# Kernel tuning notes

Hardware: AMD Instinct MI355X
Metric: run time of the kernel (lower is better)

## Reference

```python
import jax, jax.numpy as jnp
import numpy as np

D = 1024
H = 4096  # int(dim * mlp_ratio)
E = 8
B, N = 2, 2048


def setup_inputs() -> dict:
    key = jax.random.key(0)
    ks = jax.random.split(key, 5)
    x = jax.random.normal(ks[0], (B, N, D), dtype=jnp.float32)
    # torch Linear weights, stored pre-transposed for right-multiplication
    W1 = jax.random.normal(ks[1], (E, D, H), dtype=jnp.float32) / np.sqrt(D)
    W2 = jax.random.normal(ks[2], (E, H, D), dtype=jnp.float32) / np.sqrt(H)
    Wg = jax.random.normal(ks[3], (D, E), dtype=jnp.float32) / np.sqrt(D)
    bg = jax.random.normal(ks[4], (E,), dtype=jnp.float32) * 0.01
    return {"x": x, "W1": W1, "W2": W2, "Wg": Wg, "bg": bg}


def reference(x, W1, W2, Wg, bg):
    b, n, d = x.shape
    e = Wg.shape[1]
    xf = x.reshape(b * n, d)                      # [T, D]
    logits = xf @ Wg + bg                         # [T, E]
    one_hot = jax.nn.one_hot(jnp.argmax(logits, axis=-1), e, dtype=x.dtype)  # [T, E]
    # Dense all-experts compute (faithful to the original module)
    h = jax.nn.gelu(jnp.einsum('td,edh->eth', xf, W1), approximate=True)     # [E, T, H]
    y = jnp.einsum('eth,ehd->etd', h, W2)                                    # [E, T, D]
    out = jnp.einsum('etd,te->td', y, one_hot)                               # top-1 combine
    return out.reshape(b, n, d)
```

## Files before the change

kernel.cpp:

```cpp
#include <hip/hip_runtime.h>
#include <hip/hip_bf16.h>

#define Dq 1024
#define Hq 4096
#define Tq 4096
#define MAXTILES 40
#define BM 128
#define BN 256
#define BK 32

#define XB_OFF 65536
#define HC_OFF (XB_OFF + Tq * Dq * 2)
#define WT_OFF (HC_OFF + MAXTILES * BM * Hq * 2)

#define M_NT 0
#define M_CNT 8
#define M_POFF 16
#define M_CUR 32
#define M_TE 64
#define M_TR 128
#define M_EXP 512
#define M_PERM 4608

typedef __attribute__((ext_vector_type(8))) short bf16x8;
typedef __attribute__((ext_vector_type(4))) float f32x4;

__device__ __forceinline__ short f2bf(float f) {
    __hip_bfloat16 h = __float2bfloat16(f);
    return *reinterpret_cast<short*>(&h);
}

__device__ __forceinline__ float gelu_tanh(float x) {
    float u = 0.7978845608028654f * (x + 0.044715f * x * x * x);
    return x / (1.0f + __expf(-2.0f * u));
}

typedef __attribute__((address_space(1))) const void gvoid;
typedef __attribute__((address_space(3))) void lvoid;
__device__ __forceinline__ void glds16(const void* g, void* l) {
    __builtin_amdgcn_global_load_lds((gvoid*)g, (lvoid*)l, 16, 0, 0);
}

#define WAITVM_(N) asm volatile("s_waitcnt vmcnt(" #N ")" ::: "memory")
#define WAITVM(N) WAITVM_(N)

__global__ void k_init(int* meta) {
    int i = blockIdx.x * 256 + threadIdx.x;
    if (i < M_PERM + MAXTILES * BM) meta[i] = 0;
}

__global__ void k_tr(const float* __restrict__ in, short* __restrict__ out, int R, int C) {
    __shared__ float t[64][65];
    int e = blockIdx.z;
    int c0 = blockIdx.x * 64;
    int r0 = blockIdx.y * 64;
    const float* ine = in + (size_t)e * R * C;
    short* oute = out + (size_t)e * R * C;
    int tt = threadIdx.x;
    int lr = tt >> 4;
    int lc = (tt & 15) * 4;
#pragma unroll
    for (int p = 0; p < 4; ++p) {
        int r = p * 16 + lr;
        float4 v = *(const float4*)(ine + (size_t)(r0 + r) * C + c0 + lc);
        t[r][lc] = v.x; t[r][lc + 1] = v.y; t[r][lc + 2] = v.z; t[r][lc + 3] = v.w;
    }
    __syncthreads();
#pragma unroll
    for (int p = 0; p < 4; ++p) {
        int c = p * 16 + lr;
        short4 s;
        s.x = f2bf(t[lc][c]); s.y = f2bf(t[lc + 1][c]);
        s.z = f2bf(t[lc + 2][c]); s.w = f2bf(t[lc + 3][c]);
        *(short4*)(oute + (size_t)(c0 + c) * R + r0 + lc) = s;
    }
}

__global__ void k_route(const float* __restrict__ x, const float* __restrict__ Wg,
                        const float* __restrict__ bg, int* meta, short* __restrict__ xb) {
    int wave = threadIdx.x >> 6;
    int lane = threadIdx.x & 63;
    int t = blockIdx.x * 4 + wave;
    const float* xr = x + (size_t)t * Dq;
    float acc[8];
#pragma unroll
    for (int e = 0; e < 8; ++e) acc[e] = 0.0f;
#pragma unroll
    for (int j = 0; j < 16; ++j) {
        int d = j * 64 + lane;
        float xv = xr[d];
        xb[(size_t)t * Dq + d] = f2bf(xv);
        float4 w0 = *(const float4*)(Wg + (size_t)d * 8);
        float4 w1 = *(const float4*)(Wg + (size_t)d * 8 + 4);
        acc[0] += xv * w0.x; acc[1] += xv * w0.y; acc[2] += xv * w0.z; acc[3] += xv * w0.w;
        acc[4] += xv * w1.x; acc[5] += xv * w1.y; acc[6] += xv * w1.z; acc[7] += xv * w1.w;
    }
#pragma unroll
    for (int e = 0; e < 8; ++e) {
#pragma unroll
        for (int off = 32; off > 0; off >>= 1) acc[e] += __shfl_xor(acc[e], off);
    }
    if (lane == 0) {
        float best = acc[0] + bg[0];
        int be = 0;
#pragma unroll
        for (int e = 1; e < 8; ++e) {
            float v = acc[e] + bg[e];
            if (v > best) { best = v; be = e; }
        }
        meta[M_EXP + t] = be;
        atomicAdd(&meta[M_CNT + be], 1);
    }
}

__global__ void k_scan(int* meta) {
    if (threadIdx.x != 0) return;
    int off = 0, nt = 0;
    for (int e = 0; e < 8; ++e) {
        meta[M_POFF + e] = off;
        int c = meta[M_CNT + e];
        int m = (c + BM - 1) / BM;
        for (int j = 0; j < m; ++j) {
            meta[M_TE + nt] = e;
            meta[M_TR + nt] = off + j * BM;
            ++nt;
        }
        off += m * BM;
    }
    meta[M_POFF + 8] = off;
    meta[M_NT] = nt;
}

__global__ void k_scatter(int* meta) {
    int t = blockIdx.x * 256 + threadIdx.x;
    if (t >= Tq) return;
    int e = meta[M_EXP + t];
    int pos = atomicAdd(&meta[M_CUR + e], 1);
    meta[M_PERM + meta[M_POFF + e] + pos] = t;
}

#define GSTEP(VMN, DO_ISSUE, KN)                                               \
  {                                                                            \
    if (DO_ISSUE) {                                                            \
      int fA = fill * (BM * BK), fB = fill * (BN * BK);                        \
      glds16(aSrc + (size_t)(KN) * BK, As + fA + tt * 8);                      \
      glds16(bSrc0 + (size_t)(KN) * BK, Bs + fB + tt * 8);                     \
      glds16(bSrc1 + (size_t)(KN) * BK, Bs + fB + 4096 + tt * 8);              \
    }                                                                          \
    WAITVM(VMN);                                                               \
    __builtin_amdgcn_s_barrier();                                              \
    asm volatile("" ::: "memory");                                             \
    __builtin_amdgcn_sched_barrier(0);                                         \
    {                                                                          \
      int cA = cur * (BM * BK), cB = cur * (BN * BK);                          \
      bf16x8 af[4], bfv[4];                                                    \
      _Pragma("unroll")                                                        \
      for (int f = 0; f < 4; ++f) {                                            \
        af[f]  = *(const bf16x8*)(&As[cA + aoff[f]]);                          \
        bfv[f] = *(const bf16x8*)(&Bs[cB + boff[f]]);                          \
      }                                                                        \
      __builtin_amdgcn_s_setprio(1);                                           \
      _Pragma("unroll")                                                        \
      for (int fm = 0; fm < 4; ++fm)                                           \
        _Pragma("unroll")                                                      \
        for (int fn = 0; fn < 4; ++fn)                                         \
          acc[fm][fn] = __builtin_amdgcn_mfma_f32_16x16x32_bf16(               \
              af[fm], bfv[fn], acc[fm][fn], 0, 0, 0);                          \
      __builtin_amdgcn_s_setprio(0);                                           \
    }                                                                          \
    __builtin_amdgcn_s_barrier();                                              \
    asm volatile("" ::: "memory");                                             \
    cur = cur == 2 ? 0 : cur + 1;                                              \
    fill = fill == 2 ? 0 : fill + 1;                                           \
  }

__global__ __launch_bounds__(512, 4) void k_gemm1(const short* __restrict__ xb,
                                                  const short* __restrict__ W1T,
                                                  const int* __restrict__ meta,
                                                  short* __restrict__ Hc) {
    __shared__ short As[3 * BM * BK];
    __shared__ short Bs[3 * BN * BK];
    int lin = blockIdx.x + gridDim.x * blockIdx.y;
    int swzid = (lin & 7) * 80 + (lin >> 3);
    int mt = swzid % MAXTILES;
    int n0 = (swzid / MAXTILES) * BN;
    if (mt >= meta[M_NT]) return;
    int e = meta[M_TE + mt];
    int i0 = meta[M_TR + mt];
    int tt = threadIdx.x;
    int wave = tt >> 6, lane = tt & 63;
    int fr = lane & 15, fg = lane >> 4;
    const int* perm = meta + M_PERM;

    int am = tt >> 2;
    int asw = ((tt & 3) ^ ((am >> 1) & 3)) * 8;
    const short* aSrc = xb + (size_t)perm[i0 + am] * Dq + asw;
    int bn_ = tt >> 2;
    int bsw = ((tt & 3) ^ ((bn_ >> 1) & 3)) * 8;
    const short* bSrc0 = W1T + ((size_t)e * Hq + n0 + bn_) * Dq + bsw;
    const short* bSrc1 = bSrc0 + (size_t)128 * Dq;

    int wm = (wave >> 2) * 64, wn = (wave & 3) * 64;
    int aoff[4], boff[4];
#pragma unroll
    for (int f = 0; f < 4; ++f) {
        int m = wm + f * 16 + fr;
        aoff[f] = m * BK + ((fg ^ ((m >> 1) & 3)) * 8);
        int n = wn + f * 16 + fr;
        boff[f] = n * BK + ((fg ^ ((n >> 1) & 3)) * 8);
    }

    f32x4 acc[4][4];
#pragma unroll
    for (int a = 0; a < 4; ++a)
#pragma unroll
        for (int b = 0; b < 4; ++b) acc[a][b] = (f32x4){0.f, 0.f, 0.f, 0.f};

    glds16(aSrc, As + tt * 8);
    glds16(bSrc0, Bs + tt * 8);
    glds16(bSrc1, Bs + 4096 + tt * 8);
    glds16(aSrc + BK, As + BM * BK + tt * 8);
    glds16(bSrc0 + BK, Bs + BN * BK + tt * 8);
    glds16(bSrc1 + BK, Bs + BN * BK + 4096 + tt * 8);

    int cur = 0, fill = 2;
    for (int i = 0; i < 30; ++i) GSTEP(6, true, i + 2)
    GSTEP(3, false, 0)
    GSTEP(0, false, 0)

#pragma unroll
    for (int fm = 0; fm < 4; ++fm) {
        int rbase = i0 + wm + fm * 16 + fg * 4;
#pragma unroll
        for (int fn = 0; fn < 4; ++fn) {
            int col = n0 + wn + fn * 16 + fr;
#pragma unroll
            for (int q = 0; q < 4; ++q) {
                float v = gelu_tanh(acc[fm][fn][q]);
                Hc[(size_t)(rbase + q) * Hq + col] = f2bf(v);
            }
        }
    }
}

__global__ __launch_bounds__(512, 4) void k_gemm2(const short* __restrict__ Hc,
                                                  const short* __restrict__ W2T,
                                                  const int* __restrict__ meta,
                                                  float* __restrict__ out) {
    __shared__ short As[3 * BM * BK];
    __shared__ short Bs[3 * BN * BK];
    int lin = blockIdx.x + 40 * (blockIdx.y + 4 * blockIdx.z);
    int swzid = (lin & 7) * 40 + (lin >> 3);
    int mt = swzid % MAXTILES;
    int rest = swzid / MAXTILES;
    int n0 = (rest & 3) * BN;
    int kbase = (rest >> 2) * (Hq / 2);
    if (mt >= meta[M_NT]) return;
    int e = meta[M_TE + mt];
    int i0 = meta[M_TR + mt];
    int tt = threadIdx.x;
    int wave = tt >> 6, lane = tt & 63;
    int fr = lane & 15, fg = lane >> 4;
    const int* perm = meta + M_PERM;
    int vend = meta[M_POFF + e] + meta[M_CNT + e];

    int am = tt >> 2;
    int asw = ((tt & 3) ^ ((am >> 1) & 3)) * 8;
    const short* aSrc = Hc + (size_t)(i0 + am) * Hq + kbase + asw;
    int bn_ = tt >> 2;
    int bsw = ((tt & 3) ^ ((bn_ >> 1) & 3)) * 8;
    const short* bSrc0 = W2T + ((size_t)e * Dq + n0 + bn_) * Hq + kbase + bsw;
    const short* bSrc1 = bSrc0 + (size_t)128 * Hq;

    int wm = (wave >> 2) * 64, wn = (wave & 3) * 64;
    int aoff[4], boff[4];
#pragma unroll
    for (int f = 0; f < 4; ++f) {
        int m = wm + f * 16 + fr;
        aoff[f] = m * BK + ((fg ^ ((m >> 1) & 3)) * 8);
        int n = wn + f * 16 + fr;
        boff[f] = n * BK + ((fg ^ ((n >> 1) & 3)) * 8);
    }

    f32x4 acc[4][4];
#pragma unroll
    for (int a = 0; a < 4; ++a)
#pragma unroll
        for (int b = 0; b < 4; ++b) acc[a][b] = (f32x4){0.f, 0.f, 0.f, 0.f};

    glds16(aSrc, As + tt * 8);
    glds16(bSrc0, Bs + tt * 8);
    glds16(bSrc1, Bs + 4096 + tt * 8);
    glds16(aSrc + BK, As + BM * BK + tt * 8);
    glds16(bSrc0 + BK, Bs + BN * BK + tt * 8);
    glds16(bSrc1 + BK, Bs + BN * BK + 4096 + tt * 8);

    int cur = 0, fill = 2;
    for (int i = 0; i < 62; ++i) GSTEP(6, true, i + 2)
    GSTEP(3, false, 0)
    GSTEP(0, false, 0)

#pragma unroll
    for (int fm = 0; fm < 4; ++fm) {
        int rbase = i0 + wm + fm * 16 + fg * 4;
#pragma unroll
        for (int q = 0; q < 4; ++q) {
            int i = rbase + q;
            if (i < vend) {
                int tok = perm[i];
#pragma unroll
                for (int fn = 0; fn < 4; ++fn) {
                    int col = n0 + wn + fn * 16 + fr;
                    atomicAdd(&out[(size_t)tok * Dq + col], acc[fm][fn][q]);
                }
            }
        }
    }
}

extern "C" void kernel_launch(void* const* d_in, const int* in_sizes, int n_in,
                              void* d_out, int out_size, void* d_ws, size_t ws_size,
                              hipStream_t stream) {
    const float* x  = (const float*)d_in[0];
    const float* W1 = (const float*)d_in[1];
    const float* W2 = (const float*)d_in[2];
    const float* Wg = (const float*)d_in[3];
    const float* bg = (const float*)d_in[4];
    float* out = (float*)d_out;
    int* meta = (int*)d_ws;
    short* xb = (short*)((char*)d_ws + XB_OFF);
    short* Hc = (short*)((char*)d_ws + HC_OFF);
    short* WT = (short*)((char*)d_ws + WT_OFF);

    k_init<<<38, 256, 0, stream>>>(meta);
    hipMemsetAsync(d_out, 0, (size_t)Tq * Dq * 4, stream);
    k_route<<<Tq / 4, 256, 0, stream>>>(x, Wg, bg, meta, xb);
    k_scan<<<1, 64, 0, stream>>>(meta);
    k_scatter<<<Tq / 256, 256, 0, stream>>>(meta);
    k_tr<<<dim3(Hq / 64, Dq / 64, 8), 256, 0, stream>>>(W1, WT, Dq, Hq);
    dim3 g1(MAXTILES, Hq / BN);
    k_gemm1<<<g1, 512, 0, stream>>>(xb, WT, meta, Hc);
    k_tr<<<dim3(Dq / 64, Hq / 64, 8), 256, 0, stream>>>(W2, WT, Hq, Dq);
    dim3 g2(MAXTILES, Dq / BN, 2);
    k_gemm2<<<g2, 512, 0, stream>>>(Hc, WT, meta, out);
}
```

Measured before the change: 312.6 us.

## Fuse fp32 weight transpose-convert into GEMM B-tile loading, drop k_tr passes

Removes the two separate transpose-and-convert kernels that turned W1/W2 into bf16 transposed copies. Instead, each GEMM block reads fp32 weight rows straight into registers, converts them to bf16 and writes them into a swizzled LDS tile, overlapping the next tile's loads with the current tile's compute. Tiles change to 128x128 with BK=64, 256 threads and double buffering. This saves a full read and write of the weights per call, but adds conversion work and register pressure inside the GEMM main loop, and the fp32 B reads now cost twice the bandwidth of the bf16 copies.

```diff
diff --git a/kernel.cpp b/kernel.cpp
--- a/kernel.cpp
+++ b/kernel.cpp
@@ -5,13 +5,9 @@
 #define Hq 4096
 #define Tq 4096
 #define MAXTILES 40
-#define BM 128
-#define BN 256
-#define BK 32
 
 #define XB_OFF 65536
 #define HC_OFF (XB_OFF + Tq * Dq * 2)
-#define WT_OFF (HC_OFF + MAXTILES * BM * Hq * 2)
 
 #define M_NT 0
 #define M_CNT 8
@@ -46,34 +42,7 @@
 
 __global__ void k_init(int* meta) {
     int i = blockIdx.x * 256 + threadIdx.x;
-    if (i < M_PERM + MAXTILES * BM) meta[i] = 0;
-}
-
-__global__ void k_tr(const float* __restrict__ in, short* __restrict__ out, int R, int C) {
-    __shared__ float t[64][65];
-    int e = blockIdx.z;
-    int c0 = blockIdx.x * 64;
-    int r0 = blockIdx.y * 64;
-    const float* ine = in + (size_t)e * R * C;
-    short* oute = out + (size_t)e * R * C;
-    int tt = threadIdx.x;
-    int lr = tt >> 4;
-    int lc = (tt & 15) * 4;
-#pragma unroll
-    for (int p = 0; p < 4; ++p) {
-        int r = p * 16 + lr;
-        float4 v = *(const float4*)(ine + (size_t)(r0 + r) * C + c0 + lc);
-        t[r][lc] = v.x; t[r][lc + 1] = v.y; t[r][lc + 2] = v.z; t[r][lc + 3] = v.w;
-    }
-    __syncthreads();
-#pragma unroll
-    for (int p = 0; p < 4; ++p) {
-        int c = p * 16 + lr;
-        short4 s;
-        s.x = f2bf(t[lc][c]); s.y = f2bf(t[lc + 1][c]);
-        s.z = f2bf(t[lc + 2][c]); s.w = f2bf(t[lc + 3][c]);
-        *(short4*)(oute + (size_t)(c0 + c) * R + r0 + lc) = s;
-    }
+    if (i < M_PERM + MAXTILES * 128) meta[i] = 0;
 }
 
 __global__ void k_route(const float* __restrict__ x, const float* __restrict__ Wg,
@@ -119,13 +88,13 @@
     for (int e = 0; e < 8; ++e) {
         meta[M_POFF + e] = off;
         int c = meta[M_CNT + e];
-        int m = (c + BM - 1) / BM;
+        int m = (c + 127) / 128;
         for (int j = 0; j < m; ++j) {
             meta[M_TE + nt] = e;
-            meta[M_TR + nt] = off + j * BM;
+            meta[M_TR + nt] = off + j * 128;
             ++nt;
         }
-        off += m * BM;
+        off += m * 128;
     }
     meta[M_POFF + 8] = off;
     meta[M_NT] = nt;
@@ -139,25 +108,37 @@
     meta[M_PERM + meta[M_POFF + e] + pos] = t;
 }
 
-#define GSTEP(VMN, DO_ISSUE, KN)                                               \
+#define STEP(RC, RN, P, ISS, KN, LDB)                                          \
   {                                                                            \
-    if (DO_ISSUE) {                                                            \
-      int fA = fill * (BM * BK), fB = fill * (BN * BK);                        \
-      glds16(aSrc + (size_t)(KN) * BK, As + fA + tt * 8);                      \
-      glds16(bSrc0 + (size_t)(KN) * BK, Bs + fB + tt * 8);                     \
-      glds16(bSrc1 + (size_t)(KN) * BK, Bs + fB + 4096 + tt * 8);              \
+    if (ISS) {                                                                 \
+      _Pragma("unroll")                                                        \
+      for (int s = 0; s < 4; ++s)                                              \
+        glds16(aSrc[s] + (size_t)(KN) * 64, As + (1 - (P)) * 8192 + ldsA[s]);  \
+      _Pragma("unroll")                                                        \
+      for (int r = 0; r < 8; ++r)                                              \
+        RN[r] = *(const float4*)(bSrc + ((size_t)(KN) * 64 + r) * (LDB));      \
+      WAITVM(12);                                                              \
+    } else {                                                                   \
+      WAITVM(0);                                                               \
     }                                                                          \
-    WAITVM(VMN);                                                               \
+    _Pragma("unroll")                                                          \
+    for (int j = 0; j < 4; ++j) {                                              \
+      bf16x8 v;                                                                \
+      _Pragma("unroll")                                                        \
+      for (int r = 0; r < 8; ++r) v[r] = f2bf(((const float*)&RC[r])[j]);      \
+      *(bf16x8*)(Bs + (P) * 8192 + bwoff[j]) = v;                              \
+    }                                                                          \
+    asm volatile("s_waitcnt lgkmcnt(0)" ::: "memory");                         \
     __builtin_amdgcn_s_barrier();                                              \
     asm volatile("" ::: "memory");                                             \
     __builtin_amdgcn_sched_barrier(0);                                         \
-    {                                                                          \
-      int cA = cur * (BM * BK), cB = cur * (BN * BK);                          \
+    _Pragma("unroll")                                                          \
+    for (int s2 = 0; s2 < 2; ++s2) {                                           \
       bf16x8 af[4], bfv[4];                                                    \
       _Pragma("unroll")                                                        \
       for (int f = 0; f < 4; ++f) {                                            \
-        af[f]  = *(const bf16x8*)(&As[cA + aoff[f]]);                          \
-        bfv[f] = *(const bf16x8*)(&Bs[cB + boff[f]]);                          \
+        af[f]  = *(const bf16x8*)(&As[(P) * 8192 + aoff[s2][f]]);              \
+        bfv[f] = *(const bf16x8*)(&Bs[(P) * 8192 + boff[s2][f]]);              \
       }                                                                        \
       __builtin_amdgcn_s_setprio(1);                                           \
       _Pragma("unroll")                                                        \
@@ -170,63 +151,76 @@
     }                                                                          \
     __builtin_amdgcn_s_barrier();                                              \
     asm volatile("" ::: "memory");                                             \
-    cur = cur == 2 ? 0 : cur + 1;                                              \
-    fill = fill == 2 ? 0 : fill + 1;                                           \
   }
 
-__global__ __launch_bounds__(512, 4) void k_gemm1(const short* __restrict__ xb,
-                                                  const short* __restrict__ W1T,
+#define GEMM_SETUP()                                                           \
+    int tt = threadIdx.x, w = tt >> 6, lane = tt & 63;                         \
+    int fr = lane & 15, fg = lane >> 4;                                        \
+    int rlo = lane >> 3, csw = (lane & 7) ^ rlo;                               \
+    int ldsA[4];                                                               \
+    _Pragma("unroll")                                                          \
+    for (int s = 0; s < 4; ++s) ldsA[s] = (s * 32 + w * 8) * 64;               \
+    int n4 = (tt & 31) * 4, kb = (tt >> 5) * 8;                                \
+    int bwoff[4];                                                              \
+    _Pragma("unroll")                                                          \
+    for (int j = 0; j < 4; ++j) {                                              \
+      int n = n4 + j;                                                          \
+      bwoff[j] = n * 64 + (((kb >> 3) ^ ((n + (n >> 3)) & 7)) * 8);            \
+    }                                                                          \
+    int wm = (w >> 1) * 64, wn = (w & 1) * 64;                                 \
+    int aoff[2][4], boff[2][4];                                                \
+    _Pragma("unroll")                                                          \
+    for (int s2 = 0; s2 < 2; ++s2)                                             \
+      _Pragma("unroll")                                                        \
+      for (int f = 0; f < 4; ++f) {                                            \
+        int c = s2 * 4 + fg;                                                   \
+        int m = wm + f * 16 + fr;                                              \
+        aoff[s2][f] = m * 64 + ((c ^ (m & 7)) * 8);                            \
+        int n = wn + f * 16 + fr;                                              \
+        boff[s2][f] = n * 64 + ((c ^ ((n + (n >> 3)) & 7)) * 8);               \
+      }                                                                        \
+    f32x4 acc[4][4];                                                           \
+    _Pragma("unroll")                                                          \
+    for (int a = 0; a < 4; ++a)                                                \
+      _Pragma("unroll")                                                        \
+      for (int b = 0; b < 4; ++b) acc[a][b] = (f32x4){0.f, 0.f, 0.f, 0.f};
+
+__global__ __launch_bounds__(256, 2) void k_gemm1(const short* __restrict__ xb,
+                                                  const float* __restrict__ W1,
                                                   const int* __restrict__ meta,
                                                   short* __restrict__ Hc) {
-    __shared__ short As[3 * BM * BK];
-    __shared__ short Bs[3 * BN * BK];
-    int lin = blockIdx.x + gridDim.x * blockIdx.y;
-    int swzid = (lin & 7) * 80 + (lin >> 3);
-    int mt = swzid % MAXTILES;
-    int n0 = (swzid / MAXTILES) * BN;
+    __shared__ short As[2 * 128 * 64];
+    __shared__ short Bs[2 * 128 * 64];
+    int hw = blockIdx.x;
+    int swzid = (hw & 7) * 160 + (hw >> 3);
+    int q = swzid % 160;
+    int mt = q >> 2;
+    int n0 = ((swzid / 160) * 4 + (q & 3)) * 128;
     if (mt >= meta[M_NT]) return;
     int e = meta[M_TE + mt];
     int i0 = meta[M_TR + mt];
-    int tt = threadIdx.x;
-    int wave = tt >> 6, lane = tt & 63;
-    int fr = lane & 15, fg = lane >> 4;
     const int* perm = meta + M_PERM;
 
-    int am = tt >> 2;
-    int asw = ((tt & 3) ^ ((am >> 1) & 3)) * 8;
-    const short* aSrc = xb + (size_t)perm[i0 + am] * Dq + asw;
-    int bn_ = tt >> 2;
-    int bsw = ((tt & 3) ^ ((bn_ >> 1) & 3)) * 8;
-    const short* bSrc0 = W1T + ((size_t)e * Hq + n0 + bn_) * Dq + bsw;
-    const short* bSrc1 = bSrc0 + (size_t)128 * Dq;
-
-    int wm = (wave >> 2) * 64, wn = (wave & 3) * 64;
-    int aoff[4], boff[4];
-#pragma unroll
-    for (int f = 0; f < 4; ++f) {
-        int m = wm + f * 16 + fr;
-        aoff[f] = m * BK + ((fg ^ ((m >> 1) & 3)) * 8);
-        int n = wn + f * 16 + fr;
-        boff[f] = n * BK + ((fg ^ ((n >> 1) & 3)) * 8);
-    }
-
-    f32x4 acc[4][4];
-#pragma unroll
-    for (int a = 0; a < 4; ++a)
-#pragma unroll
-        for (int b = 0; b < 4; ++b) acc[a][b] = (f32x4){0.f, 0.f, 0.f, 0.f};
-
-    glds16(aSrc, As + tt * 8);
-    glds16(bSrc0, Bs + tt * 8);
-    glds16(bSrc1, Bs + 4096 + tt * 8);
-    glds16(aSrc + BK, As + BM * BK + tt * 8);
-    glds16(bSrc0 + BK, Bs + BN * BK + tt * 8);
-    glds16(bSrc1 + BK, Bs + BN * BK + 4096 + tt * 8);
-
-    int cur = 0, fill = 2;
-    for (int i = 0; i < 30; ++i) GSTEP(6, true, i + 2)
-    GSTEP(3, false, 0)
-    GSTEP(0, false, 0)
+    GEMM_SETUP()
+
+    const short* aSrc[4];
+#pragma unroll
+    for (int s = 0; s < 4; ++s) {
+        int row = s * 32 + w * 8 + rlo;
+        aSrc[s] = xb + (size_t)perm[i0 + row] * Dq + csw * 8;
+    }
+    const float* bSrc = W1 + ((size_t)e * Dq + kb) * Hq + n0 + n4;
+
+    float4 rB0[8], rB1[8];
+#pragma unroll
+    for (int s = 0; s < 4; ++s) glds16(aSrc[s], As + ldsA[s]);
+#pragma unroll
+    for (int r = 0; r < 8; ++r) rB0[r] = *(const float4*)(bSrc + (size_t)r * Hq);
+
+    for (int t = 0; t < 16; t += 2) {
+        STEP(rB0, rB1, 0, true, t + 1, Hq)
+        STEP(rB1, rB0, 1, (t + 2) < 16, t + 2, Hq)
+    }
 
 #pragma unroll
     for (int fm = 0; fm < 4; ++fm) {
@@ -235,83 +229,65 @@
         for (int fn = 0; fn < 4; ++fn) {
             int col = n0 + wn + fn * 16 + fr;
 #pragma unroll
-            for (int q = 0; q < 4; ++q) {
-                float v = gelu_tanh(acc[fm][fn][q]);
-                Hc[(size_t)(rbase + q) * Hq + col] = f2bf(v);
+            for (int p = 0; p < 4; ++p) {
+                float v = gelu_tanh(acc[fm][fn][p]);
+                Hc[(size_t)(rbase + p) * Hq + col] = f2bf(v);
             }
         }
     }
 }
 
-__global__ __launch_bounds__(512, 4) void k_gemm2(const short* __restrict__ Hc,
-                                                  const short* __restrict__ W2T,
+__global__ __launch_bounds__(256, 2) void k_gemm2(const short* __restrict__ Hc,
+                                                  const float* __restrict__ W2,
                                                   const int* __restrict__ meta,
                                                   float* __restrict__ out) {
-    __shared__ short As[3 * BM * BK];
-    __shared__ short Bs[3 * BN * BK];
-    int lin = blockIdx.x + 40 * (blockIdx.y + 4 * blockIdx.z);
-    int swzid = (lin & 7) * 40 + (lin >> 3);
-    int mt = swzid % MAXTILES;
-    int rest = swzid / MAXTILES;
-    int n0 = (rest & 3) * BN;
-    int kbase = (rest >> 2) * (Hq / 2);
+    __shared__ short As[2 * 128 * 64];
+    __shared__ short Bs[2 * 128 * 64];
+    int hw = blockIdx.x;
+    int swzid = (hw & 7) * 80 + (hw >> 3);
+    int q = swzid % 80;
+    int mt = q >> 1;
+    int kbase = (q & 1) * (Hq / 2);
+    int n0 = (swzid / 80) * 128;
     if (mt >= meta[M_NT]) return;
     int e = meta[M_TE + mt];
     int i0 = meta[M_TR + mt];
-    int tt = threadIdx.x;
-    int wave = tt >> 6, lane = tt & 63;
-    int fr = lane & 15, fg = lane >> 4;
     const int* perm = meta + M_PERM;
     int vend = meta[M_POFF + e] + meta[M_CNT + e];
 
-    int am = tt >> 2;
-    int asw = ((tt & 3) ^ ((am >> 1) & 3)) * 8;
-    const short* aSrc = Hc + (size_t)(i0 + am) * Hq + kbase + asw;
-    int bn_ = tt >> 2;
-    int bsw = ((tt & 3) ^ ((bn_ >> 1) & 3)) * 8;
-    const short* bSrc0 = W2T + ((size_t)e * Dq + n0 + bn_) * Hq + kbase + bsw;
-    const short* bSrc1 = bSrc0 + (size_t)128 * Hq;
-
-    int wm = (wave >> 2) * 64, wn = (wave & 3) * 64;
-    int aoff[4], boff[4];
-#pragma unroll
-    for (int f = 0; f < 4; ++f) {
-        int m = wm + f * 16 + fr;
-        aoff[f] = m * BK + ((fg ^ ((m >> 1) & 3)) * 8);
-        int n = wn + f * 16 + fr;
-        boff[f] = n * BK + ((fg ^ ((n >> 1) & 3)) * 8);
-    }
-
-    f32x4 acc[4][4];
-#pragma unroll
-    for (int a = 0; a < 4; ++a)
-#pragma unroll
-        for (int b = 0; b < 4; ++b) acc[a][b] = (f32x4){0.f, 0.f, 0.f, 0.f};
-
-    glds16(aSrc, As + tt * 8);
-    glds16(bSrc0, Bs + tt * 8);
-    glds16(bSrc1, Bs + 4096 + tt * 8);
-    glds16(aSrc + BK, As + BM * BK + tt * 8);
-    glds16(bSrc0 + BK, Bs + BN * BK + tt * 8);
-    glds16(bSrc1 + BK, Bs + BN * BK + 4096 + tt * 8);
-
-    int cur = 0, fill = 2;
-    for (int i = 0; i < 62; ++i) GSTEP(6, true, i + 2)
-    GSTEP(3, false, 0)
-    GSTEP(0, false, 0)
+    GEMM_SETUP()
+
+    const short* aSrc[4];
+#pragma unroll
+    for (int s = 0; s < 4; ++s) {
+        int row = s * 32 + w * 8 + rlo;
+        aSrc[s] = Hc + (size_t)(i0 + row) * Hq + kbase + csw * 8;
+    }
+    const float* bSrc = W2 + ((size_t)e * Hq + kbase + kb) * Dq + n0 + n4;
+
+    float4 rB0[8], rB1[8];
+#pragma unroll
+    for (int s = 0; s < 4; ++s) glds16(aSrc[s], As + ldsA[s]);
+#pragma unroll
+    for (int r = 0; r < 8; ++r) rB0[r] = *(const float4*)(bSrc + (size_t)r * Dq);
+
+    for (int t = 0; t < 32; t += 2) {
+        STEP(rB0, rB1, 0, true, t + 1, Dq)
+        STEP(rB1, rB0, 1, (t + 2) < 32, t + 2, Dq)
+    }
 
 #pragma unroll
     for (int fm = 0; fm < 4; ++fm) {
         int rbase = i0 + wm + fm * 16 + fg * 4;
 #pragma unroll
-        for (int q = 0; q < 4; ++q) {
-            int i = rbase + q;
+        for (int p = 0; p < 4; ++p) {
+            int i = rbase + p;
             if (i < vend) {
                 int tok = perm[i];
 #pragma unroll
                 for (int fn = 0; fn < 4; ++fn) {
                     int col = n0 + wn + fn * 16 + fr;
-                    atomicAdd(&out[(size_t)tok * Dq + col], acc[fm][fn][q]);
+                    atomicAdd(&out[(size_t)tok * Dq + col], acc[fm][fn][p]);
                 }
             }
         }
@@ -330,17 +306,12 @@
     int* meta = (int*)d_ws;
     short* xb = (short*)((char*)d_ws + XB_OFF);
     short* Hc = (short*)((char*)d_ws + HC_OFF);
-    short* WT = (short*)((char*)d_ws + WT_OFF);
 
     k_init<<<38, 256, 0, stream>>>(meta);
     hipMemsetAsync(d_out, 0, (size_t)Tq * Dq * 4, stream);
     k_route<<<Tq / 4, 256, 0, stream>>>(x, Wg, bg, meta, xb);
     k_scan<<<1, 64, 0, stream>>>(meta);
     k_scatter<<<Tq / 256, 256, 0, stream>>>(meta);
-    k_tr<<<dim3(Hq / 64, Dq / 64, 8), 256, 0, stream>>>(W1, WT, Dq, Hq);
-    dim3 g1(MAXTILES, Hq / BN);
-    k_gemm1<<<g1, 512, 0, stream>>>(xb, WT, meta, Hc);
-    k_tr<<<dim3(Dq / 64, Hq / 64, 8), 256, 0, stream>>>(W2, WT, Hq, Dq);
-    dim3 g2(MAXTILES, Dq / BN, 2);
-    k_gemm2<<<g2, 512, 0, stream>>>(Hc, WT, meta, out);
-}
+    k_gemm1<<<1280, 256, 0, stream>>>(xb, W1, meta, Hc);
+    k_gemm2<<<640, 256, 0, stream>>>(Hc, W2, meta, out);
+}
```

After: 286.3 us, median of 3. 8.4% less time.
